# Performance work log

Measured on AMD Instinct MI355X. Metric: run time of the kernel, lower is better.

## Reference

```python
import jax, jax.numpy as jnp
import numpy as np

N_NODES = 50000
N_EDGES = 500000
D = 128
VOCAB = 10000
OUT = 64
LAYERS = 3
N_GRAPHS = 512


def setup_inputs() -> dict:
    key = jax.random.key(0)
    ks = jax.random.split(key, 10)
    nodes = jax.random.randint(ks[0], (N_NODES,), 0, VOCAB)
    edges = jax.random.randint(ks[1], (2, N_EDGES), 0, N_NODES)
    indices = jax.random.randint(ks[2], (N_NODES,), 0, N_GRAPHS)
    emb = jax.random.normal(ks[3], (VOCAB, D), dtype=jnp.float32) * 0.02
    W0 = jax.random.normal(ks[4], (LAYERS, D, D), dtype=jnp.float32) * (1.0 / np.sqrt(D))
    W1 = jax.random.normal(ks[5], (LAYERS, D, D), dtype=jnp.float32) * (1.0 / np.sqrt(D))
    W2 = jax.random.normal(ks[6], (LAYERS, D, D), dtype=jnp.float32) * (1.0 / np.sqrt(D))
    Wout = jax.random.normal(ks[7], (2 * D, OUT), dtype=jnp.float32) * (1.0 / np.sqrt(2 * D))
    bout = jnp.zeros((OUT,), dtype=jnp.float32)
    return {"nodes": nodes, "edges": edges, "indices": indices, "num_graphs": N_GRAPHS,
            "emb": emb, "W0": W0, "W1": W1, "W2": W2, "Wout": Wout, "bout": bout}


def reference(nodes, edges, indices, num_graphs, emb, W0, W1, W2, Wout, bout):
    n = nodes.shape[0]
    h = emb[nodes]  # [N, D]; Dropout(0.5) is identity in eval mode
    src, dst = edges[0], edges[1]
    seg = jnp.concatenate([dst, src])  # message destinations, [2E]
    deg = jax.ops.segment_sum(jnp.ones_like(seg, dtype=h.dtype), seg, num_segments=n)
    deg = jnp.maximum(deg, 1.0)[:, None]
    for l in range(W0.shape[0]):
        # per-edge linear on gathered endpoints (nn.Linear: x @ W.T)
        m = jnp.concatenate([h[src] @ W1[l].T, h[dst] @ W2[l].T], axis=0)  # [2E, D]
        msg = jax.ops.segment_sum(m, seg, num_segments=n) / deg  # scatter_mean
        h = jax.nn.relu(h @ W0[l].T + msg)
    # graph pooling: scatter_mean + scatter_max
    cnt = jax.ops.segment_sum(jnp.ones((n,), h.dtype), indices, num_segments=num_graphs)
    mean = jax.ops.segment_sum(h, indices, num_segments=num_graphs) / jnp.maximum(cnt, 1.0)[:, None]
    mx = jax.ops.segment_max(h, indices, num_segments=num_graphs)
    mx = jnp.where(jnp.isfinite(mx), mx, 0.0)  # empty segments -> 0 (torch_scatter default)
    v = jnp.concatenate([mean, mx], axis=1)  # [G, 2D]
    return v @ Wout + bout
```

## Files before the change

### kernel.cpp

```cpp
#include <hip/hip_runtime.h>
#include <hip/hip_bf16.h>

#define D 128
#define GRAPHS 512
#define OUTD 64

typedef _Float16 half4v __attribute__((ext_vector_type(4)));
typedef _Float16 half8v __attribute__((ext_vector_type(8)));
typedef float float4v __attribute__((ext_vector_type(4)));
typedef float float8v __attribute__((ext_vector_type(8)));

__global__ void prep_kernel(const int* __restrict__ nodes, const float* __restrict__ emb,
                            _Float16* __restrict__ h,
                            const int* __restrict__ edges, const int* __restrict__ indices,
                            int* cnt_in, int* cnt_out, int* gcnt,
                            const float* __restrict__ W0, const float* __restrict__ W1,
                            const float* __restrict__ W2, _Float16* __restrict__ Wpk,
                            int E, int n) {
    int i = blockIdx.x * 256 + threadIdx.x;
    if (i < n * 32) {
        int v = i >> 5, q = i & 31;
        float4 f = ((const float4*)emb)[nodes[v] * 32 + q];
        half4v o = {(_Float16)f.x, (_Float16)f.y, (_Float16)f.z, (_Float16)f.w};
        ((half4v*)h)[i] = o;
    }
    if (i < E) {
        atomicAdd(&cnt_out[edges[i]], 1);
        atomicAdd(&cnt_in[edges[E + i]], 1);
    }
    if (i < n) atomicAdd(&gcnt[indices[i]], 1);
    if (i < 36864) {
        int j4 = (i & 1) * 4;
        int t = i >> 1;
        int lane = t & 63; t >>= 6;
        int nf = t & 7;   t >>= 3;
        int ks = t & 3;   t >>= 2;
        int src = t % 3;
        int l = t / 3;
        const float* W = (src == 0 ? W0 : (src == 1 ? W1 : W2)) + l * D * D;
        int col = nf * 16 + (lane & 15);
        int k = ks * 32 + (lane >> 4) * 8 + j4;
        float4 f = *(const float4*)&W[col * D + k];
        half4v o = {(_Float16)f.x, (_Float16)f.y, (_Float16)f.z, (_Float16)f.w};
        _Float16* dst = Wpk + ((size_t)(((l * 3 + src) * 4 + ks) * 8 + nf) * 64 + lane) * 8 + j4;
        *(half4v*)dst = o;
    }
}

__global__ __launch_bounds__(256) void offsets_kernel(
    const int* __restrict__ c_in, int* __restrict__ o_in,
    const int* __restrict__ c_out, int* __restrict__ o_out,
    const int* __restrict__ c_g, int* __restrict__ o_g,
    int* totals, int n) {
    __shared__ int ws[8];
    int tid = threadIdx.x;
    int lane = tid & 63, wid = tid >> 6;
    int i = blockIdx.x * 256 + tid;

#define SCAN_ALLOC(cnt, off, total, len)                                   \
    do {                                                                   \
        int v_ = (i < (len)) ? (cnt)[i] : 0;                               \
        int orig_ = v_;                                                    \
        _Pragma("unroll") for (int d_ = 1; d_ < 64; d_ <<= 1) {            \
            int t_ = __shfl_up(v_, d_, 64);                                \
            if (lane >= d_) v_ += t_;                                      \
        }                                                                  \
        if (lane == 63) ws[wid] = v_;                                      \
        __syncthreads();                                                   \
        if (tid == 0) {                                                    \
            int s_ = 0;                                                    \
            for (int k_ = 0; k_ < 4; ++k_) { int t_ = ws[k_]; ws[k_] = s_; s_ += t_; } \
            ws[4] = atomicAdd((total), s_);                                \
        }                                                                  \
        __syncthreads();                                                   \
        if (i < (len)) (off)[i] = ws[4] + ws[wid] + v_ - orig_;            \
        __syncthreads();                                                   \
    } while (0)

    SCAN_ALLOC(c_in, o_in, &totals[0], n);
    SCAN_ALLOC(c_out, o_out, &totals[1], n);
    if (blockIdx.x < (GRAPHS + 255) / 256) SCAN_ALLOC(c_g, o_g, &totals[2], GRAPHS);
#undef SCAN_ALLOC
}

__global__ void fill_kernel(const int* __restrict__ edges, const int* __restrict__ indices,
                            const int* __restrict__ off_in, const int* __restrict__ off_out,
                            const int* __restrict__ goff,
                            int* cur_in, int* cur_out, int* gcur,
                            int* csr_in, int* csr_out, int* glist, int E, int n) {
    int e = blockIdx.x * 256 + threadIdx.x;
    if (e < E) {
        int s = edges[e];
        int d = edges[E + e];
        int p = atomicAdd(&cur_in[d], 1);
        csr_in[off_in[d] + p] = s;
        int q = atomicAdd(&cur_out[s], 1);
        csr_out[off_out[s] + q] = d;
    }
    if (e < n) {
        int g = indices[e];
        int p = atomicAdd(&gcur[g], 1);
        glist[goff[g] + p] = e;
    }
}

__global__ __launch_bounds__(256) void aggregate_kernel(
    const _Float16* __restrict__ h,
    const int* __restrict__ csr_in, const int* __restrict__ off_in, const int* __restrict__ cnt_in,
    const int* __restrict__ csr_out, const int* __restrict__ off_out, const int* __restrict__ cnt_out,
    _Float16* __restrict__ agg1, _Float16* __restrict__ agg2, int n) {
    int grp = threadIdx.x >> 4;
    int lane = threadIdx.x & 15;
    int v = blockIdx.x * 16 + grp;
    if (v >= n) return;
    int s1 = off_in[v], c1 = cnt_in[v];
    int s2 = off_out[v], c2 = cnt_out[v];
    float invd = 1.0f / fmaxf((float)(c1 + c2), 1.0f);
    const half8v* h8 = (const half8v*)h;

    float8v a1 = {0.f, 0.f, 0.f, 0.f, 0.f, 0.f, 0.f, 0.f};
    int i = 0;
    for (; i + 4 <= c1; i += 4) {
        int u0 = csr_in[s1 + i], u1 = csr_in[s1 + i + 1];
        int u2 = csr_in[s1 + i + 2], u3 = csr_in[s1 + i + 3];
        half8v p0 = h8[u0 * 16 + lane];
        half8v p1 = h8[u1 * 16 + lane];
        half8v p2 = h8[u2 * 16 + lane];
        half8v p3 = h8[u3 * 16 + lane];
        a1 += (__builtin_convertvector(p0, float8v) + __builtin_convertvector(p1, float8v)) +
              (__builtin_convertvector(p2, float8v) + __builtin_convertvector(p3, float8v));
    }
    for (; i < c1; ++i)
        a1 += __builtin_convertvector(h8[csr_in[s1 + i] * 16 + lane], float8v);

    float8v a2 = {0.f, 0.f, 0.f, 0.f, 0.f, 0.f, 0.f, 0.f};
    i = 0;
    for (; i + 4 <= c2; i += 4) {
        int u0 = csr_out[s2 + i], u1 = csr_out[s2 + i + 1];
        int u2 = csr_out[s2 + i + 2], u3 = csr_out[s2 + i + 3];
        half8v p0 = h8[u0 * 16 + lane];
        half8v p1 = h8[u1 * 16 + lane];
        half8v p2 = h8[u2 * 16 + lane];
        half8v p3 = h8[u3 * 16 + lane];
        a2 += (__builtin_convertvector(p0, float8v) + __builtin_convertvector(p1, float8v)) +
              (__builtin_convertvector(p2, float8v) + __builtin_convertvector(p3, float8v));
    }
    for (; i < c2; ++i)
        a2 += __builtin_convertvector(h8[csr_out[s2 + i] * 16 + lane], float8v);

    a1 *= invd;
    a2 *= invd;
    ((half8v*)agg1)[v * 16 + lane] = __builtin_convertvector(a1, half8v);
    ((half8v*)agg2)[v * 16 + lane] = __builtin_convertvector(a2, half8v);
}

__global__ __launch_bounds__(128) void transform_mfma(
    const _Float16* __restrict__ Xh, const _Float16* __restrict__ A1,
    const _Float16* __restrict__ A2, const _Float16* __restrict__ Wl,
    _Float16* __restrict__ Hout, int n) {
    __shared__ _Float16 Hs[64][136];
    int tid = threadIdx.x;
    int w = tid >> 6, lane = tid & 63;
    int rbase = blockIdx.x * 64 + w * 32;
    int m0 = lane & 15;
    int kg = lane >> 4;
    int r0 = min(rbase + m0, n - 1);
    int r1 = min(rbase + 16 + m0, n - 1);

    const _Float16* srcs[3] = {Xh, A1, A2};

    float4v acc[2][8];
#pragma unroll
    for (int mf = 0; mf < 2; ++mf)
#pragma unroll
        for (int nf = 0; nf < 8; ++nf) acc[mf][nf] = (float4v){0.f, 0.f, 0.f, 0.f};

#define LOAD_STEP(stp, A0v, A1v, Bv)                                              \
    do {                                                                          \
        const int src_ = (stp) >> 2, ks_ = (stp) & 3;                             \
        const _Float16* X_ = srcs[src_];                                          \
        A0v = *(const half8v*)(X_ + (size_t)r0 * D + ks_ * 32 + kg * 8);          \
        A1v = *(const half8v*)(X_ + (size_t)r1 * D + ks_ * 32 + kg * 8);          \
        const _Float16* wp_ = Wl + (size_t)((src_ * 4 + ks_) * 8) * 512 + lane * 8; \
        _Pragma("unroll") for (int nf_ = 0; nf_ < 8; ++nf_)                       \
            Bv[nf_] = *(const half8v*)(wp_ + nf_ * 512);                          \
    } while (0)

    half8v a0c, a1c, bc[8], a0n, a1n, bn[8];
    LOAD_STEP(0, a0c, a1c, bc);
#pragma unroll
    for (int step = 0; step < 12; ++step) {
        if (step < 11) LOAD_STEP(step + 1, a0n, a1n, bn);
#pragma unroll
        for (int nf = 0; nf < 8; ++nf) {
            acc[0][nf] = __builtin_amdgcn_mfma_f32_16x16x32_f16(a0c, bc[nf], acc[0][nf], 0, 0, 0);
            acc[1][nf] = __builtin_amdgcn_mfma_f32_16x16x32_f16(a1c, bc[nf], acc[1][nf], 0, 0, 0);
        }
        a0c = a0n; a1c = a1n;
#pragma unroll
        for (int nf = 0; nf < 8; ++nf) bc[nf] = bn[nf];
    }
#undef LOAD_STEP

#pragma unroll
    for (int mf = 0; mf < 2; ++mf)
#pragma unroll
        for (int nf = 0; nf < 8; ++nf)
#pragma unroll
            for (int r = 0; r < 4; ++r) {
                int row = w * 32 + mf * 16 + kg * 4 + r;
                int col = nf * 16 + m0;
                Hs[row][col] = (_Float16)fmaxf(acc[mf][nf][r], 0.0f);
            }
    __syncthreads();
#pragma unroll
    for (int it = 0; it < 8; ++it) {
        int id = tid + it * 128;
        int row = id >> 4, c8 = id & 15;
        int grow = blockIdx.x * 64 + row;
        if (grow < n)
            *(half8v*)(Hout + (size_t)grow * D + c8 * 8) = *(const half8v*)&Hs[row][c8 * 8];
    }
}

__global__ __launch_bounds__(128) void pool_head_kernel(
    const _Float16* __restrict__ h, const int* __restrict__ glist,
    const int* __restrict__ goff, const int* __restrict__ gcnt,
    const float* __restrict__ Wout, const float* __restrict__ bout,
    float* __restrict__ out) {
    __shared__ float feat[2 * D];
    int g = blockIdx.x;
    int t = threadIdx.x;
    int s = goff[g], c = gcnt[g];
    float sum = 0.0f, mx = 0.0f;
    int i = 0;
    for (; i + 4 <= c; i += 4) {
        int v0 = glist[s + i], v1 = glist[s + i + 1];
        int v2 = glist[s + i + 2], v3 = glist[s + i + 3];
        float a = (float)h[(size_t)v0 * D + t];
        float b = (float)h[(size_t)v1 * D + t];
        float cc = (float)h[(size_t)v2 * D + t];
        float d = (float)h[(size_t)v3 * D + t];
        sum += (a + b) + (cc + d);
        mx = fmaxf(mx, fmaxf(fmaxf(a, b), fmaxf(cc, d)));
    }
    for (; i < c; ++i) {
        float a = (float)h[(size_t)glist[s + i] * D + t];
        sum += a;
        mx = fmaxf(mx, a);
    }
    feat[t] = sum / fmaxf((float)c, 1.0f);
    feat[D + t] = mx;
    __syncthreads();
    if (t < OUTD) {
        float acc = bout[t];
#pragma unroll 8
        for (int k = 0; k < 2 * D; ++k)
            acc = fmaf(feat[k], Wout[k * OUTD + t], acc);
        out[g * OUTD + t] = acc;
    }
}

extern "C" void kernel_launch(void* const* d_in, const int* in_sizes, int n_in,
                              void* d_out, int out_size, void* d_ws, size_t ws_size,
                              hipStream_t stream) {
    const int* nodes   = (const int*)d_in[0];
    const int* edges   = (const int*)d_in[1];
    const int* indices = (const int*)d_in[2];
    const float* emb  = (const float*)d_in[4];
    const float* W0   = (const float*)d_in[5];
    const float* W1   = (const float*)d_in[6];
    const float* W2   = (const float*)d_in[7];
    const float* Wout = (const float*)d_in[8];
    const float* bout = (const float*)d_in[9];
    float* out = (float*)d_out;

    const int n = in_sizes[0];
    const int E = in_sizes[1] / 2;

    char* ws = (char*)d_ws;
    size_t off = 0;
    auto alloc = [&](size_t bytes) -> char* {
        char* p = ws + off;
        off = (off + bytes + 255) & ~(size_t)255;
        return p;
    };
    int* cnt_in  = (int*)alloc(n * sizeof(int));
    int* cnt_out = (int*)alloc(n * sizeof(int));
    int* cur_in  = (int*)alloc(n * sizeof(int));
    int* cur_out = (int*)alloc(n * sizeof(int));
    int* gcnt    = (int*)alloc(GRAPHS * sizeof(int));
    int* gcur    = (int*)alloc(GRAPHS * sizeof(int));
    int* totals  = (int*)alloc(3 * sizeof(int));
    size_t zbytes = off;
    int* off_in  = (int*)alloc(n * sizeof(int));
    int* off_out = (int*)alloc(n * sizeof(int));
    int* goff    = (int*)alloc(GRAPHS * sizeof(int));
    int* glist   = (int*)alloc(n * sizeof(int));
    int* csr_in  = (int*)alloc(E * sizeof(int));
    int* csr_out = (int*)alloc(E * sizeof(int));
    _Float16* Wpk = (_Float16*)alloc(3 * 3 * 4 * 8 * 64 * 8 * sizeof(_Float16));
    _Float16* B0 = (_Float16*)alloc((size_t)n * D * sizeof(_Float16));
    _Float16* B1 = (_Float16*)alloc((size_t)n * D * sizeof(_Float16));
    _Float16* B2 = (_Float16*)alloc((size_t)n * D * sizeof(_Float16));
    (void)ws_size;

    hipMemsetAsync(d_ws, 0, zbytes, stream);

    int pblocks = (n * 32 + 255) / 256;
    prep_kernel<<<pblocks, 256, 0, stream>>>(nodes, emb, B0, edges, indices,
                                             cnt_in, cnt_out, gcnt, W0, W1, W2, Wpk, E, n);
    int oblocks = (n + 255) / 256;
    offsets_kernel<<<oblocks, 256, 0, stream>>>(cnt_in, off_in, cnt_out, off_out,
                                                gcnt, goff, totals, n);
    int eblocks = (E + 255) / 256;
    fill_kernel<<<eblocks, 256, 0, stream>>>(edges, indices, off_in, off_out, goff,
                                             cur_in, cur_out, gcur, csr_in, csr_out, glist, E, n);

    int ablocks = (n + 15) / 16;
    int tblocks = (n + 63) / 64;
    for (int l = 0; l < 3; ++l) {
        aggregate_kernel<<<ablocks, 256, 0, stream>>>(B0, csr_in, off_in, cnt_in,
                                                      csr_out, off_out, cnt_out, B1, B2, n);
        transform_mfma<<<tblocks, 128, 0, stream>>>(B0, B1, B2,
                                                    Wpk + (size_t)l * 3 * 4 * 8 * 512,
                                                    B0, n);
    }

    pool_head_kernel<<<GRAPHS, 128, 0, stream>>>(B0, glist, goff, gcnt, Wout, bout, out);
}
```

Measured before the change: 372.0 us.

## Store CSR indices as 16-bit and move embedding/weight prep into fill kernel

Node indices in the CSR adjacency lists and the graph node list are now stored as unsigned 16-bit values instead of 32-bit ints, halving index traffic in the aggregation and pooling kernels. The embedding gather and weight packing move out of the histogram kernel into a merged fill kernel, so the histogram pass only launches as many blocks as there are edges. Node ids reach 49999, which fits in 16 bits, but the code breaks silently if the node count ever exceeds 65535.

Result: no change. 369.6 us (-0.6%).

```diff
diff --git a/kernel.cpp b/kernel.cpp
--- a/kernel.cpp
+++ b/kernel.cpp
@@ -9,42 +9,16 @@
 typedef _Float16 half8v __attribute__((ext_vector_type(8)));
 typedef float float4v __attribute__((ext_vector_type(4)));
 typedef float float8v __attribute__((ext_vector_type(8)));
-
-__global__ void prep_kernel(const int* __restrict__ nodes, const float* __restrict__ emb,
-                            _Float16* __restrict__ h,
-                            const int* __restrict__ edges, const int* __restrict__ indices,
-                            int* cnt_in, int* cnt_out, int* gcnt,
-                            const float* __restrict__ W0, const float* __restrict__ W1,
-                            const float* __restrict__ W2, _Float16* __restrict__ Wpk,
-                            int E, int n) {
+typedef unsigned short u16;
+
+__global__ void hist_kernel(const int* __restrict__ edges, const int* __restrict__ indices,
+                            int* cnt_in, int* cnt_out, int* gcnt, int E, int n) {
     int i = blockIdx.x * 256 + threadIdx.x;
-    if (i < n * 32) {
-        int v = i >> 5, q = i & 31;
-        float4 f = ((const float4*)emb)[nodes[v] * 32 + q];
-        half4v o = {(_Float16)f.x, (_Float16)f.y, (_Float16)f.z, (_Float16)f.w};
-        ((half4v*)h)[i] = o;
-    }
     if (i < E) {
         atomicAdd(&cnt_out[edges[i]], 1);
         atomicAdd(&cnt_in[edges[E + i]], 1);
     }
     if (i < n) atomicAdd(&gcnt[indices[i]], 1);
-    if (i < 36864) {
-        int j4 = (i & 1) * 4;
-        int t = i >> 1;
-        int lane = t & 63; t >>= 6;
-        int nf = t & 7;   t >>= 3;
-        int ks = t & 3;   t >>= 2;
-        int src = t % 3;
-        int l = t / 3;
-        const float* W = (src == 0 ? W0 : (src == 1 ? W1 : W2)) + l * D * D;
-        int col = nf * 16 + (lane & 15);
-        int k = ks * 32 + (lane >> 4) * 8 + j4;
-        float4 f = *(const float4*)&W[col * D + k];
-        half4v o = {(_Float16)f.x, (_Float16)f.y, (_Float16)f.z, (_Float16)f.w};
-        _Float16* dst = Wpk + ((size_t)(((l * 3 + src) * 4 + ks) * 8 + nf) * 64 + lane) * 8 + j4;
-        *(half4v*)dst = o;
-    }
 }
 
 __global__ __launch_bounds__(256) void offsets_kernel(
@@ -83,31 +57,59 @@
 #undef SCAN_ALLOC
 }
 
-__global__ void fill_kernel(const int* __restrict__ edges, const int* __restrict__ indices,
+__global__ void mega_kernel(const int* __restrict__ nodes, const float* __restrict__ emb,
+                            _Float16* __restrict__ h,
+                            const int* __restrict__ edges, const int* __restrict__ indices,
                             const int* __restrict__ off_in, const int* __restrict__ off_out,
                             const int* __restrict__ goff,
                             int* cur_in, int* cur_out, int* gcur,
-                            int* csr_in, int* csr_out, int* glist, int E, int n) {
-    int e = blockIdx.x * 256 + threadIdx.x;
-    if (e < E) {
-        int s = edges[e];
-        int d = edges[E + e];
+                            u16* __restrict__ csr_in, u16* __restrict__ csr_out,
+                            u16* __restrict__ glist,
+                            const float* __restrict__ W0, const float* __restrict__ W1,
+                            const float* __restrict__ W2, _Float16* __restrict__ Wpk,
+                            int E, int n) {
+    int i = blockIdx.x * 256 + threadIdx.x;
+    if (i < n * 32) {
+        int v = i >> 5, q = i & 31;
+        float4 f = ((const float4*)emb)[nodes[v] * 32 + q];
+        half4v o = {(_Float16)f.x, (_Float16)f.y, (_Float16)f.z, (_Float16)f.w};
+        ((half4v*)h)[i] = o;
+    }
+    if (i < E) {
+        int s = edges[i];
+        int d = edges[E + i];
         int p = atomicAdd(&cur_in[d], 1);
-        csr_in[off_in[d] + p] = s;
+        csr_in[off_in[d] + p] = (u16)s;
         int q = atomicAdd(&cur_out[s], 1);
-        csr_out[off_out[s] + q] = d;
-    }
-    if (e < n) {
-        int g = indices[e];
+        csr_out[off_out[s] + q] = (u16)d;
+    }
+    if (i < n) {
+        int g = indices[i];
         int p = atomicAdd(&gcur[g], 1);
-        glist[goff[g] + p] = e;
+        glist[goff[g] + p] = (u16)i;
+    }
+    if (i < 36864) {
+        int j4 = (i & 1) * 4;
+        int t = i >> 1;
+        int lane = t & 63; t >>= 6;
+        int nf = t & 7;   t >>= 3;
+        int ks = t & 3;   t >>= 2;
+        int src = t % 3;
+        int l = t / 3;
+        const float* W = (src == 0 ? W0 : (src == 1 ? W1 : W2)) + l * D * D;
+        int col = nf * 16 + (lane & 15);
+        int k = ks * 32 + (lane >> 4) * 8 + j4;
+        float4 f = *(const float4*)&W[col * D + k];
+        half4v o = {(_Float16)f.x, (_Float16)f.y, (_Float16)f.z, (_Float16)f.w};
+        _Float16* dst = Wpk + ((size_t)(((l * 3 + src) * 4 + ks) * 8 + nf) * 64 + lane) * 8 + j4;
+        *(half4v*)dst = o;
     }
 }
 
 __global__ __launch_bounds__(256) void aggregate_kernel(
     const _Float16* __restrict__ h,
-    const int* __restrict__ csr_in, const int* __restrict__ off_in, const int* __restrict__ cnt_in,
-    const int* __restrict__ csr_out, const int* __restrict__ off_out, const int* __restrict__ cnt_out,
+    const u16* __restrict__ csr_in, const int* __restrict__ off_in, const int* __restrict__ cnt_in,
+    const u16* __restrict__ csr_out, const int* __restrict__ off_out, const int* __restrict__ cnt_out,
     _Float16* __restrict__ agg1, _Float16* __restrict__ agg2, int n) {
     int grp = threadIdx.x >> 4;
     int lane = threadIdx.x & 15;
@@ -224,7 +226,7 @@
 }
 
 __global__ __launch_bounds__(128) void pool_head_kernel(
-    const _Float16* __restrict__ h, const int* __restrict__ glist,
+    const _Float16* __restrict__ h, const u16* __restrict__ glist,
     const int* __restrict__ goff, const int* __restrict__ gcnt,
     const float* __restrict__ Wout, const float* __restrict__ bout,
     float* __restrict__ out) {
@@ -296,9 +298,9 @@
     int* off_in  = (int*)alloc(n * sizeof(int));
     int* off_out = (int*)alloc(n * sizeof(int));
     int* goff    = (int*)alloc(GRAPHS * sizeof(int));
-    int* glist   = (int*)alloc(n * sizeof(int));
-    int* csr_in  = (int*)alloc(E * sizeof(int));
-    int* csr_out = (int*)alloc(E * sizeof(int));
+    u16* glist   = (u16*)alloc(n * sizeof(u16));
+    u16* csr_in  = (u16*)alloc(E * sizeof(u16));
+    u16* csr_out = (u16*)alloc(E * sizeof(u16));
     _Float16* Wpk = (_Float16*)alloc(3 * 3 * 4 * 8 * 64 * 8 * sizeof(_Float16));
     _Float16* B0 = (_Float16*)alloc((size_t)n * D * sizeof(_Float16));
     _Float16* B1 = (_Float16*)alloc((size_t)n * D * sizeof(_Float16));
@@ -307,15 +309,15 @@
 
     hipMemsetAsync(d_ws, 0, zbytes, stream);
 
-    int pblocks = (n * 32 + 255) / 256;
-    prep_kernel<<<pblocks, 256, 0, stream>>>(nodes, emb, B0, edges, indices,
-                                             cnt_in, cnt_out, gcnt, W0, W1, W2, Wpk, E, n);
+    int eblocks = (E + 255) / 256;
+    hist_kernel<<<eblocks, 256, 0, stream>>>(edges, indices, cnt_in, cnt_out, gcnt, E, n);
     int oblocks = (n + 255) / 256;
     offsets_kernel<<<oblocks, 256, 0, stream>>>(cnt_in, off_in, cnt_out, off_out,
                                                 gcnt, goff, totals, n);
-    int eblocks = (E + 255) / 256;
-    fill_kernel<<<eblocks, 256, 0, stream>>>(edges, indices, off_in, off_out, goff,
-                                             cur_in, cur_out, gcur, csr_in, csr_out, glist, E, n);
+    int pblocks = (n * 32 + 255) / 256;
+    mega_kernel<<<pblocks, 256, 0, stream>>>(nodes, emb, B0, edges, indices,
+                                             off_in, off_out, goff, cur_in, cur_out, gcur,
+                                             csr_in, csr_out, glist, W0, W1, W2, Wpk, E, n);
 
     int ablocks = (n + 15) / 16;
     int tblocks = (n + 63) / 64;
```
